# Kernel optimization log

Measured on AMD Instinct MI355X. Metric: run time of the kernel, lower is better.

## Reference

```python
import jax, jax.numpy as jnp
import numpy as np

CAPACITY_FACTOR = 1.25


def setup_inputs() -> dict:
    key = jax.random.key(0)
    k1, k2, k3, k4 = jax.random.split(key, 4)
    B, T, H = 2, 2048, 1024
    E, F = 8, 2048
    x = jax.random.normal(k1, (B, T, H), dtype=jnp.float32)
    Wr = jax.random.normal(k2, (H, E), dtype=jnp.float32) * 0.02
    W1 = jax.random.normal(k3, (E, H, 2 * F), dtype=jnp.float32) * 0.02
    W2 = jax.random.normal(k4, (E, F, H), dtype=jnp.float32) * 0.02
    return {"x": x, "Wr": Wr, "W1": W1, "W2": W2}


def _moe_forward(x, Wr, W1, W2):
    B, T, H = x.shape
    E = Wr.shape[1]
    N = B * T
    cap = max(1, int(CAPACITY_FACTOR * (N * 2 / E)))  # static (shape-derived)

    flat_x = x.reshape(N, H)
    logits = flat_x @ Wr                      # [N, E] (train=False: no noise)
    gate = jax.nn.softmax(logits, axis=-1)
    top2_val, top2_idx = jax.lax.top_k(gate, 2)   # [N,2]

    # --- capacity bookkeeping, matching the torch sequential fill order ---
    e0, e1 = top2_idx[:, 0], top2_idx[:, 1]
    oh0 = jax.nn.one_hot(e0, E, dtype=jnp.int32)  # [N,E]
    oh1 = jax.nn.one_hot(e1, E, dtype=jnp.int32)
    # rank of each token within its expert's k=0 queue (flattened token order)
    pos0 = jnp.take_along_axis(jnp.cumsum(oh0, axis=0), top2_idx[:, :1], axis=1)[:, 0] - 1
    count0 = oh0.sum(axis=0)                      # tokens routed top-1 per expert
    used0 = jnp.minimum(count0, cap)              # slots consumed in k=0 pass
    keep0 = pos0 < cap
    # k=1 pass starts after the slots used by k=0
    pos1 = jnp.take_along_axis(jnp.cumsum(oh1, axis=0), top2_idx[:, 1:2], axis=1)[:, 0] - 1
    pos1 = pos1 + used0[e1]
    keep1 = pos1 < cap

    dummy = E * cap  # drop slot
    slot0 = jnp.where(keep0, e0 * cap + pos0, dummy)
    slot1 = jnp.where(keep1, e1 * cap + pos1, dummy)

    # --- dispatch: [E*cap+1, H] buffer (last row is the drop slot) ---
    buf = jnp.zeros((E * cap + 1, H), dtype=x.dtype)
    buf = buf.at[slot0].set(flat_x).at[slot1].set(flat_x)
    xe = buf[: E * cap].reshape(E, cap, H)

    # --- grouped expert FFN (SwiGLU) ---
    h = jnp.einsum("ech,ehf->ecf", xe, W1)        # [E, cap, 2F]
    a, b = jnp.split(h, 2, axis=-1)
    act = jax.nn.silu(a) * b                      # [E, cap, F]
    out = jnp.einsum("ecf,efh->ech", act, W2)     # [E, cap, H]
    out_flat = out.reshape(E * cap, H)

    # --- combine: gather back per token, weighted by gate values ---
    g0 = out_flat[jnp.where(keep0, slot0, 0)] * keep0[:, None]
    g1 = out_flat[jnp.where(keep1, slot1, 0)] * keep1[:, None]
    y = g0 * top2_val[:, 0:1] + g1 * top2_val[:, 1:2]
    y = y.reshape(B, T, H)

    # --- balance loss ---
    me = 1e-9
    prob_per_expert = gate.mean(axis=0)                 # == mean over (B,T)
    used1 = (oh1 * keep1[:, None].astype(jnp.int32)).sum(axis=0)
    used = (used0 + used1).astype(gate.dtype)
    frac_used = jnp.maximum(used, me) / (N * 2 + me)
    balance_loss = (prob_per_expert * frac_used).sum() * E
    return y, balance_loss


def reference(x, Wr, W1, W2):
    return _moe_forward(x, Wr, W1, W2)
```

## Files before the change

### kernel.cpp

```cpp
#include <hip/hip_runtime.h>
#include <cstdint>

#define E_    8
#define H_    1024
#define F_    2048
#define NTOK  4096
#define CAP   1280
#define ECAP  (E_*CAP)

typedef unsigned short u16;
typedef __attribute__((ext_vector_type(8))) short bf16x8;
typedef __attribute__((ext_vector_type(4))) float f32x4;
typedef __attribute__((ext_vector_type(4))) unsigned short u16x4;

__device__ __forceinline__ u16 f2bf(float f) {
  union { float f; uint32_t u; } v; v.f = f;
  uint32_t r = v.u + 0x7fffu + ((v.u >> 16) & 1u);
  return (u16)(r >> 16);
}

__device__ __forceinline__ void gld16(const void* gsrc, void* ldst) {
  auto g = reinterpret_cast<const __attribute__((address_space(1))) uint32_t*>(
      reinterpret_cast<uintptr_t>(gsrc));
  auto l = reinterpret_cast<__attribute__((address_space(3))) uint32_t*>(
      reinterpret_cast<uintptr_t>(ldst));
  __builtin_amdgcn_global_load_lds(g, l, 16, 0, 0);
}

__device__ __forceinline__ int swz(int row, int chunk) {
  return row * 64 + ((chunk ^ (row & 7)) * 8);
}

__global__ __launch_bounds__(256) void transpose_cvt(const float* __restrict__ in,
                                                     u16* __restrict__ outp,
                                                     int R, int C) {
  __shared__ float tile[32][33];
  size_t base = (size_t)blockIdx.z * R * C;
  int r0 = blockIdx.y * 32, c0 = blockIdx.x * 32;
  int tx = threadIdx.x, ty = threadIdx.y;
#pragma unroll
  for (int i = 0; i < 4; i++)
    tile[ty + 8*i][tx] = in[base + (size_t)(r0 + ty + 8*i) * C + (c0 + tx)];
  __syncthreads();
#pragma unroll
  for (int i = 0; i < 4; i++)
    outp[base + (size_t)(c0 + ty + 8*i) * R + (r0 + tx)] = f2bf(tile[tx][ty + 8*i]);
}

__global__ __launch_bounds__(256) void router_kernel(const float* __restrict__ x,
                                                     const float* __restrict__ Wr,
                                                     int* __restrict__ e0o, int* __restrict__ e1o,
                                                     float* __restrict__ v0o, float* __restrict__ v1o,
                                                     float* __restrict__ partial) {
  int w = threadIdx.x >> 6, l = threadIdx.x & 63;
  int t = blockIdx.x * 4 + w;
  const float* xr = x + (size_t)t * H_;
  float acc[8] = {0.f,0.f,0.f,0.f,0.f,0.f,0.f,0.f};
#pragma unroll
  for (int it = 0; it < 16; ++it) {
    int h = it * 64 + l;
    float xv = xr[h];
    const float4* wr = (const float4*)(Wr + h * 8);
    float4 wa = wr[0], wb = wr[1];
    acc[0] += xv * wa.x; acc[1] += xv * wa.y; acc[2] += xv * wa.z; acc[3] += xv * wa.w;
    acc[4] += xv * wb.x; acc[5] += xv * wb.y; acc[6] += xv * wb.z; acc[7] += xv * wb.w;
  }
#pragma unroll
  for (int e = 0; e < 8; ++e)
#pragma unroll
    for (int off = 32; off; off >>= 1)
      acc[e] += __shfl_xor(acc[e], off);

  __shared__ float pg[4][8];
  if (l == 0) {
    float mx = acc[0];
#pragma unroll
    for (int e = 1; e < 8; ++e) mx = fmaxf(mx, acc[e]);
    float g[8], s = 0.f;
#pragma unroll
    for (int e = 0; e < 8; ++e) { g[e] = __expf(acc[e] - mx); s += g[e]; }
    float inv = 1.f / s;
#pragma unroll
    for (int e = 0; e < 8; ++e) g[e] *= inv;
    int b0 = 0; float m0 = g[0];
#pragma unroll
    for (int e = 1; e < 8; ++e) if (g[e] > m0) { m0 = g[e]; b0 = e; }
    int b1 = -1; float m1 = -1.f;
#pragma unroll
    for (int e = 0; e < 8; ++e) if (e != b0 && g[e] > m1) { m1 = g[e]; b1 = e; }
    e0o[t] = b0; e1o[t] = b1; v0o[t] = m0; v1o[t] = m1;
#pragma unroll
    for (int e = 0; e < 8; ++e) pg[w][e] = g[e];
  }
  __syncthreads();
  if (threadIdx.x < 8) {
    int e = threadIdx.x;
    partial[blockIdx.x * 8 + e] = pg[0][e] + pg[1][e] + pg[2][e] + pg[3][e];
  }
}

__global__ __launch_bounds__(256) void scan_kernel(const int* __restrict__ e0i, const int* __restrict__ e1i,
                                                   const float* __restrict__ partial,
                                                   int* __restrict__ slot0, int* __restrict__ slot1,
                                                   float* __restrict__ bl_out) {
  __shared__ int c0[256][8], c1[256][8];
  __shared__ float gs[256][8];
  __shared__ int used0_s[8], tot1_s[8];
  int tid = threadIdx.x;

  int le0[16], le1[16];
  int lc0[8] = {0,0,0,0,0,0,0,0}, lc1[8] = {0,0,0,0,0,0,0,0};
  for (int i = 0; i < 16; ++i) {
    int t = tid * 16 + i;
    le0[i] = e0i[t]; le1[i] = e1i[t];
    lc0[le0[i]]++; lc1[le1[i]]++;
  }
#pragma unroll
  for (int e = 0; e < 8; ++e) { c0[tid][e] = lc0[e]; c1[tid][e] = lc1[e]; }

  float g[8] = {0.f,0.f,0.f,0.f,0.f,0.f,0.f,0.f};
  for (int rr = 0; rr < 4; ++rr)
#pragma unroll
    for (int e = 0; e < 8; ++e) g[e] += partial[(tid + rr * 256) * 8 + e];
#pragma unroll
  for (int e = 0; e < 8; ++e) gs[tid][e] = g[e];
  __syncthreads();

  for (int d = 1; d < 256; d <<= 1) {
    int t0[8], t1[8];
    bool a = (tid >= d);
    if (a) {
#pragma unroll
      for (int e = 0; e < 8; ++e) { t0[e] = c0[tid - d][e]; t1[e] = c1[tid - d][e]; }
    }
    __syncthreads();
    if (a) {
#pragma unroll
      for (int e = 0; e < 8; ++e) { c0[tid][e] += t0[e]; c1[tid][e] += t1[e]; }
    }
    __syncthreads();
  }
  for (int s = 128; s > 0; s >>= 1) {
    if (tid < s)
#pragma unroll
      for (int e = 0; e < 8; ++e) gs[tid][e] += gs[tid + s][e];
    __syncthreads();
  }
  if (tid < 8) {
    int e = tid;
    used0_s[e] = min(c0[255][e], CAP);
    tot1_s[e] = c1[255][e];
  }
  __syncthreads();

  int ex0[8], ex1[8];
#pragma unroll
  for (int e = 0; e < 8; ++e) { ex0[e] = c0[tid][e] - lc0[e]; ex1[e] = c1[tid][e] - lc1[e]; }
  int r0c[8] = {0,0,0,0,0,0,0,0}, r1c[8] = {0,0,0,0,0,0,0,0};
  for (int i = 0; i < 16; ++i) {
    int t = tid * 16 + i;
    int e = le0[i];
    int pos = ex0[e] + r0c[e]; r0c[e]++;
    slot0[t] = (pos < CAP) ? (e * CAP + pos) : -1;
    e = le1[i];
    pos = ex1[e] + r1c[e] + used0_s[e]; r1c[e]++;
    slot1[t] = (pos < CAP) ? (e * CAP + pos) : -1;
  }

  if (tid == 0) {
    float bl = 0.f;
    for (int e = 0; e < 8; ++e) {
      int u1 = min(tot1_s[e], max(0, CAP - used0_s[e]));
      float used = (float)(used0_s[e] + u1);
      float fu = fmaxf(used, 1e-9f) / (8192.f + 1e-9f);
      bl += (gs[0][e] / (float)NTOK) * fu;
    }
    bl_out[0] = bl * 8.f;
  }
}

__global__ __launch_bounds__(256) void scatter_kernel(const float* __restrict__ x,
                                                      const int* __restrict__ slot0,
                                                      const int* __restrict__ slot1,
                                                      u16* __restrict__ xe) {
  int t = blockIdx.x, tid = threadIdx.x;
  float4 vv = *(const float4*)(x + (size_t)t * H_ + tid * 4);
  u16x4 b;
  b.x = f2bf(vv.x); b.y = f2bf(vv.y); b.z = f2bf(vv.z); b.w = f2bf(vv.w);
  int s0 = slot0[t], s1 = slot1[t];
  if (s0 >= 0) *(u16x4*)(xe + (size_t)s0 * H_ + tid * 4) = b;
  if (s1 >= 0) *(u16x4*)(xe + (size_t)s1 * H_ + tid * 4) = b;
}

__global__ __launch_bounds__(256, 2) void gemm1_kernel(const u16* __restrict__ xe,
                                                       const u16* __restrict__ W1T,
                                                       u16* __restrict__ act) {
  __shared__ u16 As[128 * 64];
  __shared__ u16 Bsa[64 * 64];
  __shared__ u16 Bsb[64 * 64];
  const int tid = threadIdx.x;
  const int w = tid >> 6, l = tid & 63;
  const int wm = w & 1, wn = w >> 1;
  const int mbase = blockIdx.y * 128;
  const int nbase = blockIdx.x * 64;
  const int e = mbase / 1280;
  const u16* Ap = xe + (size_t)mbase * H_;
  const u16* Ba = W1T + (size_t)e * 4096 * H_ + (size_t)nbase * H_;
  const u16* Bb = Ba + (size_t)F_ * H_;
  const int lrow = l >> 3;
  const int lcol = (((l & 7) ^ lrow) * 8);

  f32x4 acca[4][2] = {};
  f32x4 accb[4][2] = {};

  for (int kt = 0; kt < 16; ++kt) {
    int k0 = kt * 64;
#pragma unroll
    for (int r = 0; r < 4; ++r) {
      int row0 = w * 32 + r * 8;
      gld16(Ap + (size_t)(row0 + lrow) * H_ + k0 + lcol, &As[row0 * 64]);
    }
#pragma unroll
    for (int r = 0; r < 2; ++r) {
      int row0 = w * 16 + r * 8;
      gld16(Ba + (size_t)(row0 + lrow) * H_ + k0 + lcol, &Bsa[row0 * 64]);
      gld16(Bb + (size_t)(row0 + lrow) * H_ + k0 + lcol, &Bsb[row0 * 64]);
    }
    __syncthreads();
#pragma unroll
    for (int kk = 0; kk < 64; kk += 32) {
      const int ck = (kk >> 3) + (l >> 4);
      bf16x8 af[4], ba[2], bb[2];
#pragma unroll
      for (int i = 0; i < 4; ++i)
        af[i] = *(const bf16x8*)&As[swz(wm * 64 + i * 16 + (l & 15), ck)];
#pragma unroll
      for (int j = 0; j < 2; ++j) {
        ba[j] = *(const bf16x8*)&Bsa[swz(wn * 32 + j * 16 + (l & 15), ck)];
        bb[j] = *(const bf16x8*)&Bsb[swz(wn * 32 + j * 16 + (l & 15), ck)];
      }
#pragma unroll
      for (int i = 0; i < 4; ++i)
#pragma unroll
        for (int j = 0; j < 2; ++j) {
          acca[i][j] = __builtin_amdgcn_mfma_f32_16x16x32_bf16(af[i], ba[j], acca[i][j], 0, 0, 0);
          accb[i][j] = __builtin_amdgcn_mfma_f32_16x16x32_bf16(af[i], bb[j], accb[i][j], 0, 0, 0);
        }
    }
    __syncthreads();
  }
#pragma unroll
  for (int i = 0; i < 4; ++i)
#pragma unroll
    for (int j = 0; j < 2; ++j)
#pragma unroll
      for (int r = 0; r < 4; ++r) {
        int m = mbase + wm * 64 + i * 16 + (l >> 4) * 4 + r;
        int f = nbase + wn * 32 + j * 16 + (l & 15);
        float a = acca[i][j][r];
        float b = accb[i][j][r];
        float s = a / (1.f + __expf(-a));
        act[(size_t)m * F_ + f] = f2bf(s * b);
      }
}

__global__ __launch_bounds__(256, 2) void gemm2_kernel(const u16* __restrict__ act,
                                                       const u16* __restrict__ W2T,
                                                       float* __restrict__ outb) {
  __shared__ u16 As[128 * 64];
  __shared__ u16 Bs[128 * 64];
  const int tid = threadIdx.x;
  const int w = tid >> 6, l = tid & 63;
  const int wm = w & 1, wn = w >> 1;
  const int mbase = blockIdx.y * 128;
  const int nbase = blockIdx.x * 128;
  const int e = mbase / 1280;
  const u16* Ap = act + (size_t)mbase * F_;
  const u16* Bp = W2T + (size_t)e * H_ * F_ + (size_t)nbase * F_;
  const int lrow = l >> 3;
  const int lcol = (((l & 7) ^ lrow) * 8);

  f32x4 acc[4][4] = {};

  for (int kt = 0; kt < 32; ++kt) {
    int k0 = kt * 64;
#pragma unroll
    for (int r = 0; r < 4; ++r) {
      int row0 = w * 32 + r * 8;
      gld16(Ap + (size_t)(row0 + lrow) * F_ + k0 + lcol, &As[row0 * 64]);
      gld16(Bp + (size_t)(row0 + lrow) * F_ + k0 + lcol, &Bs[row0 * 64]);
    }
    __syncthreads();
#pragma unroll
    for (int kk = 0; kk < 64; kk += 32) {
      const int ck = (kk >> 3) + (l >> 4);
      bf16x8 af[4], bf[4];
#pragma unroll
      for (int i = 0; i < 4; ++i)
        af[i] = *(const bf16x8*)&As[swz(wm * 64 + i * 16 + (l & 15), ck)];
#pragma unroll
      for (int j = 0; j < 4; ++j)
        bf[j] = *(const bf16x8*)&Bs[swz(wn * 64 + j * 16 + (l & 15), ck)];
#pragma unroll
      for (int i = 0; i < 4; ++i)
#pragma unroll
        for (int j = 0; j < 4; ++j)
          acc[i][j] = __builtin_amdgcn_mfma_f32_16x16x32_bf16(af[i], bf[j], acc[i][j], 0, 0, 0);
    }
    __syncthreads();
  }
#pragma unroll
  for (int i = 0; i < 4; ++i)
#pragma unroll
    for (int j = 0; j < 4; ++j)
#pragma unroll
      for (int r = 0; r < 4; ++r) {
        int m = mbase + wm * 64 + i * 16 + (l >> 4) * 4 + r;
        int n = nbase + wn * 64 + j * 16 + (l & 15);
        outb[(size_t)m * H_ + n] = acc[i][j][r];
      }
}

__global__ __launch_bounds__(256) void combine_kernel(const float* __restrict__ outb,
                                                      const int* __restrict__ slot0,
                                                      const int* __restrict__ slot1,
                                                      const float* __restrict__ v0,
                                                      const float* __restrict__ v1,
                                                      float* __restrict__ y) {
  int t = blockIdx.x, tid = threadIdx.x;
  int s0 = slot0[t], s1 = slot1[t];
  float w0 = v0[t], w1 = v1[t];
  float4 r; r.x = 0.f; r.y = 0.f; r.z = 0.f; r.w = 0.f;
  if (s0 >= 0) {
    float4 a = *(const float4*)(outb + (size_t)s0 * H_ + tid * 4);
    r.x += w0 * a.x; r.y += w0 * a.y; r.z += w0 * a.z; r.w += w0 * a.w;
  }
  if (s1 >= 0) {
    float4 a = *(const float4*)(outb + (size_t)s1 * H_ + tid * 4);
    r.x += w1 * a.x; r.y += w1 * a.y; r.z += w1 * a.z; r.w += w1 * a.w;
  }
  *(float4*)(y + (size_t)t * H_ + tid * 4) = r;
}

#define OFF_W1T   ((size_t)0)
#define OFF_W2T   ((size_t)67108864)
#define OFF_XE    ((size_t)100663296)
#define OFF_ACT   ((size_t)121634816)
#define OFF_OUTB  ((size_t)163577856)
#define OFF_SLOT0 ((size_t)205520896)
#define OFF_SLOT1 ((size_t)205537280)
#define OFF_V0    ((size_t)205553664)
#define OFF_V1    ((size_t)205570048)
#define OFF_E0    ((size_t)205586432)
#define OFF_E1    ((size_t)205602816)
#define OFF_PART  ((size_t)205619200)

extern "C" void kernel_launch(void* const* d_in, const int* in_sizes, int n_in,
                              void* d_out, int out_size, void* d_ws, size_t ws_size,
                              hipStream_t stream) {
  const float* x  = (const float*)d_in[0];
  const float* Wr = (const float*)d_in[1];
  const float* W1 = (const float*)d_in[2];
  const float* W2 = (const float*)d_in[3];
  float* out = (float*)d_out;

  uint8_t* ws = (uint8_t*)d_ws;
  u16*   W1T   = (u16*)(ws + OFF_W1T);
  u16*   W2T   = (u16*)(ws + OFF_W2T);
  u16*   xe    = (u16*)(ws + OFF_XE);
  u16*   act   = (u16*)(ws + OFF_ACT);
  float* outb  = (float*)(ws + OFF_OUTB);
  int*   slot0 = (int*)(ws + OFF_SLOT0);
  int*   slot1 = (int*)(ws + OFF_SLOT1);
  float* v0    = (float*)(ws + OFF_V0);
  float* v1    = (float*)(ws + OFF_V1);
  int*   e0    = (int*)(ws + OFF_E0);
  int*   e1    = (int*)(ws + OFF_E1);
  float* part  = (float*)(ws + OFF_PART);

  hipMemsetAsync(xe, 0, (size_t)ECAP * H_ * sizeof(u16), stream);

  transpose_cvt<<<dim3(128, 32, 8), dim3(32, 8), 0, stream>>>(W1, W1T, H_, 2 * F_);
  transpose_cvt<<<dim3(32, 64, 8), dim3(32, 8), 0, stream>>>(W2, W2T, F_, H_);

  router_kernel<<<NTOK / 4, 256, 0, stream>>>(x, Wr, e0, e1, v0, v1, part);
  scan_kernel<<<1, 256, 0, stream>>>(e0, e1, part, slot0, slot1, out + (size_t)NTOK * H_);
  scatter_kernel<<<NTOK, 256, 0, stream>>>(x, slot0, slot1, xe);

  gemm1_kernel<<<dim3(F_ / 64, ECAP / 128), 256, 0, stream>>>(xe, W1T, act);
  gemm2_kernel<<<dim3(H_ / 128, ECAP / 128), 256, 0, stream>>>(act, W2T, outb);

  combine_kernel<<<NTOK, 256, 0, stream>>>(outb, slot0, slot1, v0, v1, out);
}
```

Measured before the change: 248.4 us.

## Double-buffer gemm1 with larger tiles, XCD-aware mapping, and vectorized transpose

gemm1 moves to 512 threads with a 256x128 output tile. It double-buffers LDS so the next K-tile's async global loads overlap MFMA compute, using explicit vmcnt waits and raw barriers instead of two __syncthreads per step. Block ids are remapped so each XCD gets a contiguous band of F tiles, which should improve L2 reuse of the weights, and s_setprio is raised around the MFMA bursts. The weight transpose-convert kernel now uses 64x64 tiles with float4 loads and 4-wide bf16 stores to cut memory-transaction overhead. The larger LDS footprint (128KB) limits gemm1 to one block per CU, and the hand-tuned waitcnts depend on the exact load count per stage.

```diff
diff --git a/kernel.cpp b/kernel.cpp
--- a/kernel.cpp
+++ b/kernel.cpp
@@ -34,17 +34,30 @@
 __global__ __launch_bounds__(256) void transpose_cvt(const float* __restrict__ in,
                                                      u16* __restrict__ outp,
                                                      int R, int C) {
-  __shared__ float tile[32][33];
+  __shared__ float tile[64][65];
   size_t base = (size_t)blockIdx.z * R * C;
-  int r0 = blockIdx.y * 32, c0 = blockIdx.x * 32;
+  int r0 = blockIdx.y * 64, c0 = blockIdx.x * 64;
   int tx = threadIdx.x, ty = threadIdx.y;
 #pragma unroll
-  for (int i = 0; i < 4; i++)
-    tile[ty + 8*i][tx] = in[base + (size_t)(r0 + ty + 8*i) * C + (c0 + tx)];
+  for (int i = 0; i < 4; i++) {
+    int row = ty + 16 * i;
+    float4 v = *(const float4*)(in + base + (size_t)(r0 + row) * C + c0 + tx * 4);
+    tile[row][tx * 4 + 0] = v.x;
+    tile[row][tx * 4 + 1] = v.y;
+    tile[row][tx * 4 + 2] = v.z;
+    tile[row][tx * 4 + 3] = v.w;
+  }
   __syncthreads();
 #pragma unroll
-  for (int i = 0; i < 4; i++)
-    outp[base + (size_t)(c0 + ty + 8*i) * R + (r0 + tx)] = f2bf(tile[tx][ty + 8*i]);
+  for (int i = 0; i < 4; i++) {
+    int c = ty + 16 * i;
+    u16x4 b;
+    b.x = f2bf(tile[tx * 4 + 0][c]);
+    b.y = f2bf(tile[tx * 4 + 1][c]);
+    b.z = f2bf(tile[tx * 4 + 2][c]);
+    b.w = f2bf(tile[tx * 4 + 3][c]);
+    *(u16x4*)(outp + base + (size_t)(c0 + c) * R + r0 + tx * 4) = b;
+  }
 }
 
 __global__ __launch_bounds__(256) void router_kernel(const float* __restrict__ x,
@@ -192,71 +205,102 @@
   if (s1 >= 0) *(u16x4*)(xe + (size_t)s1 * H_ + tid * 4) = b;
 }
 
-__global__ __launch_bounds__(256, 2) void gemm1_kernel(const u16* __restrict__ xe,
+__global__ __launch_bounds__(512, 2) void gemm1_kernel(const u16* __restrict__ xe,
                                                        const u16* __restrict__ W1T,
                                                        u16* __restrict__ act) {
-  __shared__ u16 As[128 * 64];
-  __shared__ u16 Bsa[64 * 64];
-  __shared__ u16 Bsb[64 * 64];
+  __shared__ u16 As[2][256 * 64];
+  __shared__ u16 Bsa[2][128 * 64];
+  __shared__ u16 Bsb[2][128 * 64];
+
   const int tid = threadIdx.x;
   const int w = tid >> 6, l = tid & 63;
-  const int wm = w & 1, wn = w >> 1;
-  const int mbase = blockIdx.y * 128;
-  const int nbase = blockIdx.x * 64;
-  const int e = mbase / 1280;
+  const int wm = w >> 2, wf = w & 3;
+
+  int bid = blockIdx.x;
+  int xcd = bid & 7, idx = bid >> 3;
+  int fb = xcd * 2 + idx / 40;
+  int mb = idx % 40;
+  const int mbase = mb * 256;
+  const int nbase = fb * 128;
+  const int e = mb / 5;
+
   const u16* Ap = xe + (size_t)mbase * H_;
   const u16* Ba = W1T + (size_t)e * 4096 * H_ + (size_t)nbase * H_;
   const u16* Bb = Ba + (size_t)F_ * H_;
   const int lrow = l >> 3;
   const int lcol = (((l & 7) ^ lrow) * 8);
 
-  f32x4 acca[4][2] = {};
-  f32x4 accb[4][2] = {};
-
-  for (int kt = 0; kt < 16; ++kt) {
+  f32x4 acca[8][2] = {};
+  f32x4 accb[8][2] = {};
+
+  auto STAGE = [&](int buf, int kt) {
     int k0 = kt * 64;
 #pragma unroll
     for (int r = 0; r < 4; ++r) {
       int row0 = w * 32 + r * 8;
-      gld16(Ap + (size_t)(row0 + lrow) * H_ + k0 + lcol, &As[row0 * 64]);
+      gld16(Ap + (size_t)(row0 + lrow) * H_ + k0 + lcol, &As[buf][row0 * 64]);
     }
 #pragma unroll
     for (int r = 0; r < 2; ++r) {
       int row0 = w * 16 + r * 8;
-      gld16(Ba + (size_t)(row0 + lrow) * H_ + k0 + lcol, &Bsa[row0 * 64]);
-      gld16(Bb + (size_t)(row0 + lrow) * H_ + k0 + lcol, &Bsb[row0 * 64]);
-    }
-    __syncthreads();
-#pragma unroll
-    for (int kk = 0; kk < 64; kk += 32) {
-      const int ck = (kk >> 3) + (l >> 4);
-      bf16x8 af[4], ba[2], bb[2];
-#pragma unroll
-      for (int i = 0; i < 4; ++i)
-        af[i] = *(const bf16x8*)&As[swz(wm * 64 + i * 16 + (l & 15), ck)];
+      gld16(Ba + (size_t)(row0 + lrow) * H_ + k0 + lcol, &Bsa[buf][row0 * 64]);
+      gld16(Bb + (size_t)(row0 + lrow) * H_ + k0 + lcol, &Bsb[buf][row0 * 64]);
+    }
+  };
+
+  STAGE(0, 0);
+  int cur = 0;
+
+  for (int kt = 0; kt < 16; ++kt) {
+    if (kt < 15) {
+      STAGE(cur ^ 1, kt + 1);
+      asm volatile("s_waitcnt vmcnt(8)" ::: "memory");
+    } else {
+      asm volatile("s_waitcnt vmcnt(0)" ::: "memory");
+    }
+    __builtin_amdgcn_s_barrier();
+
+    const u16* Ac = As[cur];
+    const u16* Bac = Bsa[cur];
+    const u16* Bbc = Bsb[cur];
+
+#pragma unroll
+    for (int kk = 0; kk < 2; ++kk) {
+      const int ck = kk * 4 + (l >> 4);
+      bf16x8 af[8], ba[2], bb[2];
+#pragma unroll
+      for (int i = 0; i < 8; ++i)
+        af[i] = *(const bf16x8*)&Ac[swz(wm * 128 + i * 16 + (l & 15), ck)];
 #pragma unroll
       for (int j = 0; j < 2; ++j) {
-        ba[j] = *(const bf16x8*)&Bsa[swz(wn * 32 + j * 16 + (l & 15), ck)];
-        bb[j] = *(const bf16x8*)&Bsb[swz(wn * 32 + j * 16 + (l & 15), ck)];
+        ba[j] = *(const bf16x8*)&Bac[swz(wf * 32 + j * 16 + (l & 15), ck)];
+        bb[j] = *(const bf16x8*)&Bbc[swz(wf * 32 + j * 16 + (l & 15), ck)];
       }
-#pragma unroll
-      for (int i = 0; i < 4; ++i)
+      asm volatile("s_waitcnt lgkmcnt(0)" ::: "memory");
+      __builtin_amdgcn_sched_barrier(0);
+      if (kk == 1)
+        __builtin_amdgcn_s_barrier();
+      __builtin_amdgcn_s_setprio(1);
+#pragma unroll
+      for (int i = 0; i < 8; ++i)
 #pragma unroll
         for (int j = 0; j < 2; ++j) {
           acca[i][j] = __builtin_amdgcn_mfma_f32_16x16x32_bf16(af[i], ba[j], acca[i][j], 0, 0, 0);
           accb[i][j] = __builtin_amdgcn_mfma_f32_16x16x32_bf16(af[i], bb[j], accb[i][j], 0, 0, 0);
         }
-    }
-    __syncthreads();
-  }
-#pragma unroll
-  for (int i = 0; i < 4; ++i)
+      __builtin_amdgcn_s_setprio(0);
+    }
+    cur ^= 1;
+  }
+
+#pragma unroll
+  for (int i = 0; i < 8; ++i)
 #pragma unroll
     for (int j = 0; j < 2; ++j)
 #pragma unroll
       for (int r = 0; r < 4; ++r) {
-        int m = mbase + wm * 64 + i * 16 + (l >> 4) * 4 + r;
-        int f = nbase + wn * 32 + j * 16 + (l & 15);
+        int m = mbase + wm * 128 + i * 16 + (l >> 4) * 4 + r;
+        int f = nbase + wf * 32 + j * 16 + (l & 15);
         float a = acca[i][j][r];
         float b = accb[i][j][r];
         float s = a / (1.f + __expf(-a));
@@ -380,14 +424,14 @@
 
   hipMemsetAsync(xe, 0, (size_t)ECAP * H_ * sizeof(u16), stream);
 
-  transpose_cvt<<<dim3(128, 32, 8), dim3(32, 8), 0, stream>>>(W1, W1T, H_, 2 * F_);
-  transpose_cvt<<<dim3(32, 64, 8), dim3(32, 8), 0, stream>>>(W2, W2T, F_, H_);
+  transpose_cvt<<<dim3(64, 16, 8), dim3(16, 16), 0, stream>>>(W1, W1T, H_, 2 * F_);
+  transpose_cvt<<<dim3(16, 32, 8), dim3(16, 16), 0, stream>>>(W2, W2T, F_, H_);
 
   router_kernel<<<NTOK / 4, 256, 0, stream>>>(x, Wr, e0, e1, v0, v1, part);
   scan_kernel<<<1, 256, 0, stream>>>(e0, e1, part, slot0, slot1, out + (size_t)NTOK * H_);
   scatter_kernel<<<NTOK, 256, 0, stream>>>(x, slot0, slot1, xe);
 
-  gemm1_kernel<<<dim3(F_ / 64, ECAP / 128), 256, 0, stream>>>(xe, W1T, act);
+  gemm1_kernel<<<640, 512, 0, stream>>>(xe, W1T, act);
   gemm2_kernel<<<dim3(H_ / 128, ECAP / 128), 256, 0, stream>>>(act, W2T, outb);
 
   combine_kernel<<<NTOK, 256, 0, stream>>>(outb, slot0, slot1, v0, v1, out);
```

Measured after the change: 256.2 us. 3.1% more time.
